# Kernel optimization log

Hardware: AMD Instinct MI355X
Metric: run time of the kernel (lower is better)

The kernel has to match this reference:

```python
import jax, jax.numpy as jnp
import numpy as np

N, E, C, H = 50000, 1600000, 128, 8


def setup_inputs() -> dict:
    key = jax.random.key(0)
    k1, k2, k3, k4, k5 = jax.random.split(key, 5)
    x = jax.random.normal(k1, (N, C), jnp.float32)
    row = jax.random.randint(k2, (E,), 0, N, dtype=jnp.int32)
    col = jax.random.randint(k3, (E,), 0, N, dtype=jnp.int32)
    # ensure no self loops so remove_self_loops is a static no-op
    col = jnp.where(row == col, (col + 1) % N, col)
    edge_index = jnp.stack([row, col])
    edge_attr = jax.random.normal(k4, (E,), jnp.float32)
    # Linear(2*C, H) params
    W = jax.random.normal(k5, (2 * C, H), jnp.float32) / np.sqrt(2.0 * C)
    b = jnp.zeros((H,), jnp.float32)
    return {"x": x, "edge_index": edge_index, "edge_attr": edge_attr, "W": W, "b": b}


def reference(x, edge_index, edge_attr, W, b):
    n, c = x.shape
    # add self loops (inputs contain none); PyG fill_value=1 for edge weight
    loop = jnp.arange(n, dtype=edge_index.dtype)
    row = jnp.concatenate([edge_index[0], loop])  # [E+N]
    col = jnp.concatenate([edge_index[1], loop])
    ea = jnp.concatenate([edge_attr, jnp.ones((n,), edge_attr.dtype)])
    # cat([x[row], x[col]]) @ W == x[row] @ W[:C] + x[col] @ W[C:] (avoids 2C concat buffer)
    alpha = x[row] @ W[:c] + x[col] @ W[c:] + b          # [E+N, H]
    alpha = alpha * jnp.abs(ea)[:, None]
    alpha = jax.nn.leaky_relu(alpha, negative_slope=0.2)
    alpha = alpha * 100.0
    # segment softmax grouped by row (PyG softmax)
    m = jax.ops.segment_max(alpha, row, num_segments=n)   # [N, H]
    m = jnp.where(jnp.isfinite(m), m, 0.0)                # guard empty segments
    e = jnp.exp(alpha - m[row])
    s = jax.ops.segment_sum(e, row, num_segments=n)
    alpha = e / (s[row] + 1e-16)
    return alpha, jnp.stack([row, col])
```

## Files before the change

kernel.cpp:

```cpp
#include <hip/hip_runtime.h>

#define NN 50000
#define EE 1600000
#define CC 128
#define HH 8
#define TOT (EE + NN)
#define RPB 64
#define NB  ((NN + RPB - 1) / RPB)
#define CAP 2560
#define BCH 4096
#define NBB ((EE + BCH - 1) / BCH)
#define NIT 8
#define GRIDF 4096
#define SRT 512

typedef unsigned long long ull;

__device__ inline float act(float z) {
    z = (z >= 0.f) ? z : 0.2f * z;
    return z * 100.f;
}

__global__ __launch_bounds__(256) void k_proj(const float* __restrict__ x,
                                              const float* __restrict__ W,
                                              const float* __restrict__ bias,
                                              float* __restrict__ yk,
                                              float* __restrict__ y2,
                                              int* __restrict__ gcur0) {
    if (blockIdx.x == 0) {
        for (int i = threadIdx.x; i < NB; i += 256) gcur0[i] = 0;
    }
    __shared__ float w[2 * CC * HH];
    int tid = threadIdx.x;
    for (int i = tid; i < 2 * CC * HH; i += 256) w[i] = W[i];
    __syncthreads();
    int node = blockIdx.x * 16 + (tid >> 4);
    int j = tid & 15;
    if (node >= NN) return;
    int wofs = (j < 8) ? j : (CC * HH + j - 8);
    const float4* xv = (const float4*)(x + (size_t)node * CC);
    float acc = 0.f;
#pragma unroll 4
    for (int k4 = 0; k4 < CC / 4; ++k4) {
        float4 xx = xv[k4];
        int base = k4 * 32 + wofs;
        acc += xx.x * w[base];
        acc += xx.y * w[base + 8];
        acc += xx.z * w[base + 16];
        acc += xx.w * w[base + 24];
    }
    if (j < 8) yk[(size_t)node * 16 + j] = acc + bias[j];
    else       y2[(size_t)node * 8 + (j - 8)] = acc;
}

__global__ __launch_bounds__(1024) void k_bin(const int* __restrict__ rowp,
                                              const int* __restrict__ colp,
                                              const float* __restrict__ ea,
                                              int* __restrict__ gcur0,
                                              uint2* __restrict__ pay) {
    __shared__ int hist[NB];
    __shared__ int lscan[NB];
    __shared__ int lofs[NB];
    __shared__ int gofs[NB];
    __shared__ int sc[1024];
    __shared__ uint2 stage[BCH];
    int t = threadIdx.x;
    int base = blockIdx.x * BCH;
    int n = EE - base; if (n > BCH) n = BCH;
    for (int i = t; i < NB; i += 1024) hist[i] = 0;
    __syncthreads();
    for (int i = t; i < n; i += 1024)
        atomicAdd(&hist[rowp[base + i] >> 6], 1);
    __syncthreads();
    int own = (t < NB) ? hist[t] : 0;
    sc[t] = own;
    __syncthreads();
    for (int off = 1; off < 1024; off <<= 1) {
        int v = (t >= off) ? sc[t - off] : 0;
        __syncthreads();
        sc[t] += v;
        __syncthreads();
    }
    if (t < NB) {
        int ex = sc[t] - own;
        lscan[t] = ex;
        lofs[t] = ex;
        gofs[t] = own ? (t * CAP + atomicAdd(&gcur0[t], own)) : 0;
    }
    __syncthreads();
    for (int i = t; i < n; i += 1024) {
        int r = rowp[base + i];
        int c = colp[base + i];
        float w = fabsf(ea[base + i]);
        int bkt = r >> 6;
        int p = atomicAdd(&lofs[bkt], 1);
        stage[p] = make_uint2((unsigned)(r & 63) | ((unsigned)c << 6) |
                              ((unsigned)bkt << 22),
                              __float_as_uint(w));
    }
    __syncthreads();
    for (int i = t; i < n; i += 1024) {
        uint2 v = stage[i];
        int bkt = v.x >> 22;
        int idx = gofs[bkt] + (i - lscan[bkt]);
        if (idx < (bkt + 1) * CAP)
            pay[idx] = v;
    }
}

__global__ __launch_bounds__(SRT) void k_sortrow(const int* __restrict__ gcur0,
                                                 const uint2* __restrict__ pay,
                                                 float* __restrict__ yk,
                                                 const float* __restrict__ y2,
                                                 float* __restrict__ alpha,
                                                 float* __restrict__ oidx) {
    __shared__ int cnt[RPB];
    __shared__ int rstartL[RPB + 1];
    __shared__ int ofs2[RPB];
    __shared__ uint2 stg[CAP];
    int b = blockIdx.x;
    int t = threadIdx.x;
    int s0 = b * CAP;
    int n = gcur0[b];
    if (n > CAP) n = CAP;
    if (t < RPB) cnt[t] = 0;
    __syncthreads();
    for (int i = t; i < n; i += SRT)
        atomicAdd(&cnt[pay[s0 + i].x & 63], 1);
    __syncthreads();
    if (t < RPB) {
        int v = cnt[t];
        int s = v;
        for (int off = 1; off < 64; off <<= 1) {
            int u = __shfl_up(s, off, 64);
            if (t >= off) s += u;
        }
        int ex = s - v;
        ofs2[t] = ex;
        rstartL[t] = ex;
        if (t == RPB - 1) rstartL[RPB] = s;
    }
    __syncthreads();
    for (int i = t; i < n; i += SRT) {
        uint2 p = pay[s0 + i];
        int rl = p.x & 63;
        int pos = atomicAdd(&ofs2[rl], 1);
        stg[pos] = make_uint2((p.x >> 6) & 0xFFFF, p.y);
    }
    __syncthreads();
    int wv = t >> 6;
    int lane = t & 63;
    int sub = lane >> 3;
    int h = lane & 7;
    int r0 = b * RPB;
    for (int q = 0; q < 8; ++q) {
        int rr = wv * 8 + q;
        int r = r0 + rr;
        if (r >= NN) break;
        int ls = rstartL[rr];
        int ldeg = rstartL[rr + 1] - ls;
        int tot = ldeg + 1;
        float yh = yk[(size_t)r * 16 + h];
        float y2s = y2[(size_t)r * 8 + h];
        float cache[NIT];
        float mx = -__builtin_inff();
#pragma unroll
        for (int it = 0; it < NIT; ++it) {
            int i = it * 8 + sub;
            float a = -__builtin_inff();
            if (i < ldeg) {
                uint2 p = stg[ls + i];
                a = act((yh + y2[(size_t)p.x * 8 + h]) * __uint_as_float(p.y));
            } else if (i == ldeg) {
                a = act(yh + y2s);
            }
            cache[it] = a;
            mx = fmaxf(mx, a);
        }
        for (int i = NIT * 8 + sub; i < tot; i += 8) {
            float a;
            if (i < ldeg) {
                uint2 p = stg[ls + i];
                a = act((yh + y2[(size_t)p.x * 8 + h]) * __uint_as_float(p.y));
            } else {
                a = act(yh + y2s);
            }
            mx = fmaxf(mx, a);
        }
        mx = fmaxf(mx, __shfl_xor(mx, 8, 64));
        mx = fmaxf(mx, __shfl_xor(mx, 16, 64));
        mx = fmaxf(mx, __shfl_xor(mx, 32, 64));
        float sum = 0.f;
#pragma unroll
        for (int it = 0; it < NIT; ++it)
            sum += __expf(cache[it] - mx);
        for (int i = NIT * 8 + sub; i < tot; i += 8) {
            float a;
            if (i < ldeg) {
                uint2 p = stg[ls + i];
                a = act((yh + y2[(size_t)p.x * 8 + h]) * __uint_as_float(p.y));
            } else {
                a = act(yh + y2s);
            }
            sum += __expf(a - mx);
        }
        sum += __shfl_xor(sum, 8, 64);
        sum += __shfl_xor(sum, 16, 64);
        sum += __shfl_xor(sum, 32, 64);
        if (sub == 0) {
            float K = mx + __logf(sum + 1e-16f);
            yk[(size_t)r * 16 + 8 + h] = K;
            float os = __expf(act(yh + y2s) - K);
            __builtin_nontemporal_store(os, &alpha[(size_t)(EE + r) * 8 + h]);
            if (h == 0) __builtin_nontemporal_store((float)r, &oidx[EE + r]);
            if (h == 1)
                __builtin_nontemporal_store((float)r, &oidx[(size_t)TOT + EE + r]);
        }
    }
}

__global__ __launch_bounds__(256) void k_final(const int* __restrict__ rowp,
                                               const int* __restrict__ colp,
                                               const float* __restrict__ ea,
                                               const float* __restrict__ yk,
                                               const float* __restrict__ y2,
                                               float* __restrict__ alpha,
                                               float* __restrict__ oidx) {
    int gid = blockIdx.x * 256 + threadIdx.x;
    int h = gid & 7;
    int g0 = gid >> 3;
    const int stride = (GRIDF * 256) >> 3;
    for (int e0 = g0; e0 < EE; e0 += 4 * stride) {
        int rr[4], cc[4]; float ww[4]; bool hv[4];
#pragma unroll
        for (int u = 0; u < 4; ++u) {
            int e = e0 + u * stride;
            hv[u] = e < EE;
            rr[u] = 0; cc[u] = 0; ww[u] = 0.f;
            if (hv[u]) {
                rr[u] = rowp[e];
                cc[u] = colp[e];
                ww[u] = fabsf(ea[e]);
            }
        }
        float yv[4], Kv[4], vb[4];
#pragma unroll
        for (int u = 0; u < 4; ++u) {
            yv[u] = 0.f; Kv[u] = 0.f; vb[u] = 0.f;
            if (hv[u]) {
                yv[u] = yk[(size_t)rr[u] * 16 + h];
                Kv[u] = yk[(size_t)rr[u] * 16 + 8 + h];
                vb[u] = y2[(size_t)cc[u] * 8 + h];
            }
        }
#pragma unroll
        for (int u = 0; u < 4; ++u) {
            if (hv[u]) {
                int e = e0 + u * stride;
                float o = __expf(act((yv[u] + vb[u]) * ww[u]) - Kv[u]);
                __builtin_nontemporal_store(o, &alpha[(size_t)e * 8 + h]);
                if (h == 0) __builtin_nontemporal_store((float)rr[u], &oidx[e]);
                if (h == 1)
                    __builtin_nontemporal_store((float)cc[u], &oidx[(size_t)TOT + e]);
            }
        }
    }
}

extern "C" void kernel_launch(void* const* d_in, const int* in_sizes, int n_in,
                              void* d_out, int out_size, void* d_ws, size_t ws_size,
                              hipStream_t stream) {
    const float* x    = (const float*)d_in[0];
    const int*   rowp = (const int*)d_in[1];
    const int*   colp = rowp + EE;
    const float* ea   = (const float*)d_in[2];
    const float* W    = (const float*)d_in[3];
    const float* bias = (const float*)d_in[4];

    float* out_alpha = (float*)d_out;
    float* out_idx   = out_alpha + (size_t)TOT * 8;

    float*  yk     = (float*)d_ws;
    float*  y2     = yk + (size_t)NN * 16;
    uint2*  pay    = (uint2*)(y2 + (size_t)NN * 8);
    int*    gcur0  = (int*)(pay + (size_t)NB * CAP);

    k_proj<<<(NN * 16 + 255) / 256, 256, 0, stream>>>(x, W, bias, yk, y2, gcur0);
    k_bin<<<NBB, 1024, 0, stream>>>(rowp, colp, ea, gcur0, pay);
    k_sortrow<<<NB, SRT, 0, stream>>>(gcur0, pay, yk, y2, out_alpha, out_idx);
    k_final<<<GRIDF, 256, 0, stream>>>(rowp, colp, ea, yk, y2,
                                       out_alpha, out_idx);
}
```

Baseline: 98.37 us.

## Use wave-shuffle scan in binning, stage payload in LDS, raise final unroll

The block-wide prefix scan in the binning kernel is replaced with a two-level wave-shuffle scan, cutting about twenty block barriers down to two. The row-sort kernel now copies the payload into shared memory on its first pass, so the second pass reads from LDS instead of global memory. This doubles the kernel's LDS footprint and may lower occupancy. The final edge kernel's unroll factor rises from 4 to 8 to keep more gathers in flight, at the cost of extra registers.

```diff
diff --git a/kernel.cpp b/kernel.cpp
--- a/kernel.cpp
+++ b/kernel.cpp
@@ -13,6 +13,7 @@
 #define NIT 8
 #define GRIDF 4096
 #define SRT 512
+#define UF 8
 
 typedef unsigned long long ull;
 
@@ -62,9 +63,10 @@
     __shared__ int lscan[NB];
     __shared__ int lofs[NB];
     __shared__ int gofs[NB];
-    __shared__ int sc[1024];
+    __shared__ int wsum[16];
     __shared__ uint2 stage[BCH];
     int t = threadIdx.x;
+    int lane = t & 63, wv = t >> 6;
     int base = blockIdx.x * BCH;
     int n = EE - base; if (n > BCH) n = BCH;
     for (int i = t; i < NB; i += 1024) hist[i] = 0;
@@ -73,16 +75,27 @@
         atomicAdd(&hist[rowp[base + i] >> 6], 1);
     __syncthreads();
     int own = (t < NB) ? hist[t] : 0;
-    sc[t] = own;
-    __syncthreads();
-    for (int off = 1; off < 1024; off <<= 1) {
-        int v = (t >= off) ? sc[t - off] : 0;
-        __syncthreads();
-        sc[t] += v;
-        __syncthreads();
-    }
+    int s = own;
+#pragma unroll
+    for (int off = 1; off < 64; off <<= 1) {
+        int u = __shfl_up(s, off, 64);
+        if (lane >= off) s += u;
+    }
+    if (lane == 63) wsum[wv] = s;
+    __syncthreads();
+    if (t < 16) {
+        int v = wsum[t];
+        int ss = v;
+#pragma unroll
+        for (int off = 1; off < 16; off <<= 1) {
+            int u = __shfl_up(ss, off, 16);
+            if (t >= off) ss += u;
+        }
+        wsum[t] = ss - v;
+    }
+    __syncthreads();
+    int ex = s + wsum[wv] - own;
     if (t < NB) {
-        int ex = sc[t] - own;
         lscan[t] = ex;
         lofs[t] = ex;
         gofs[t] = own ? (t * CAP + atomicAdd(&gcur0[t], own)) : 0;
@@ -117,7 +130,8 @@
     __shared__ int cnt[RPB];
     __shared__ int rstartL[RPB + 1];
     __shared__ int ofs2[RPB];
-    __shared__ uint2 stg[CAP];
+    __shared__ uint2 stgA[CAP];
+    __shared__ uint2 stgB[CAP];
     int b = blockIdx.x;
     int t = threadIdx.x;
     int s0 = b * CAP;
@@ -125,8 +139,11 @@
     if (n > CAP) n = CAP;
     if (t < RPB) cnt[t] = 0;
     __syncthreads();
-    for (int i = t; i < n; i += SRT)
-        atomicAdd(&cnt[pay[s0 + i].x & 63], 1);
+    for (int i = t; i < n; i += SRT) {
+        uint2 p = pay[s0 + i];
+        stgA[i] = p;
+        atomicAdd(&cnt[p.x & 63], 1);
+    }
     __syncthreads();
     if (t < RPB) {
         int v = cnt[t];
@@ -142,10 +159,10 @@
     }
     __syncthreads();
     for (int i = t; i < n; i += SRT) {
-        uint2 p = pay[s0 + i];
+        uint2 p = stgA[i];
         int rl = p.x & 63;
         int pos = atomicAdd(&ofs2[rl], 1);
-        stg[pos] = make_uint2((p.x >> 6) & 0xFFFF, p.y);
+        stgB[pos] = make_uint2((p.x >> 6) & 0xFFFF, p.y);
     }
     __syncthreads();
     int wv = t >> 6;
@@ -169,7 +186,7 @@
             int i = it * 8 + sub;
             float a = -__builtin_inff();
             if (i < ldeg) {
-                uint2 p = stg[ls + i];
+                uint2 p = stgB[ls + i];
                 a = act((yh + y2[(size_t)p.x * 8 + h]) * __uint_as_float(p.y));
             } else if (i == ldeg) {
                 a = act(yh + y2s);
@@ -180,7 +197,7 @@
         for (int i = NIT * 8 + sub; i < tot; i += 8) {
             float a;
             if (i < ldeg) {
-                uint2 p = stg[ls + i];
+                uint2 p = stgB[ls + i];
                 a = act((yh + y2[(size_t)p.x * 8 + h]) * __uint_as_float(p.y));
             } else {
                 a = act(yh + y2s);
@@ -197,7 +214,7 @@
         for (int i = NIT * 8 + sub; i < tot; i += 8) {
             float a;
             if (i < ldeg) {
-                uint2 p = stg[ls + i];
+                uint2 p = stgB[ls + i];
                 a = act((yh + y2[(size_t)p.x * 8 + h]) * __uint_as_float(p.y));
             } else {
                 a = act(yh + y2s);
@@ -230,10 +247,10 @@
     int h = gid & 7;
     int g0 = gid >> 3;
     const int stride = (GRIDF * 256) >> 3;
-    for (int e0 = g0; e0 < EE; e0 += 4 * stride) {
-        int rr[4], cc[4]; float ww[4]; bool hv[4];
-#pragma unroll
-        for (int u = 0; u < 4; ++u) {
+    for (int e0 = g0; e0 < EE; e0 += UF * stride) {
+        int rr[UF], cc[UF]; float ww[UF]; bool hv[UF];
+#pragma unroll
+        for (int u = 0; u < UF; ++u) {
             int e = e0 + u * stride;
             hv[u] = e < EE;
             rr[u] = 0; cc[u] = 0; ww[u] = 0.f;
@@ -243,9 +260,9 @@
                 ww[u] = fabsf(ea[e]);
             }
         }
-        float yv[4], Kv[4], vb[4];
-#pragma unroll
-        for (int u = 0; u < 4; ++u) {
+        float yv[UF], Kv[UF], vb[UF];
+#pragma unroll
+        for (int u = 0; u < UF; ++u) {
             yv[u] = 0.f; Kv[u] = 0.f; vb[u] = 0.f;
             if (hv[u]) {
                 yv[u] = yk[(size_t)rr[u] * 16 + h];
@@ -254,7 +271,7 @@
             }
         }
 #pragma unroll
-        for (int u = 0; u < 4; ++u) {
+        for (int u = 0; u < UF; ++u) {
             if (hv[u]) {
                 int e = e0 + u * stride;
                 float o = __expf(act((yv[u] + vb[u]) * ww[u]) - Kv[u]);
```

New measurement: 107.4 us. 1.09x slower.
